# Kernel tuning notes

Measured on AMD Instinct MI355X. Metric: run time of the kernel, lower is better.

## Reference

```python
import jax, jax.numpy as jnp
import numpy as np

N_NODES = 50000
N_EDGES = 1600000
EMB_DIM = 128
HIDDEN = 128   # 2 * out_channels
OUT = 64       # out_channels


def setup_inputs() -> dict:
    key = jax.random.key(0)
    ks = jax.random.split(key, 8)
    x = jnp.arange(N_NODES, dtype=jnp.int64)
    edge_index = jax.random.randint(ks[0], (2, N_EDGES), 0, N_NODES, dtype=jnp.int64)
    emb = jax.random.normal(ks[1], (N_NODES, EMB_DIM), dtype=jnp.float32) * 0.02
    W1 = jax.random.normal(ks[2], (EMB_DIM, HIDDEN), dtype=jnp.float32) / np.sqrt(EMB_DIM).astype(np.float32)
    b1 = jax.random.normal(ks[3], (HIDDEN,), dtype=jnp.float32) * 0.01
    W_mu = jax.random.normal(ks[4], (HIDDEN, OUT), dtype=jnp.float32) / np.sqrt(HIDDEN).astype(np.float32)
    b_mu = jax.random.normal(ks[5], (OUT,), dtype=jnp.float32) * 0.01
    W_logvar = jax.random.normal(ks[6], (HIDDEN, OUT), dtype=jnp.float32) / np.sqrt(HIDDEN).astype(np.float32)
    b_logvar = jax.random.normal(ks[7], (OUT,), dtype=jnp.float32) * 0.01
    return {"x": x, "edge_index": edge_index, "emb": emb, "W1": W1, "b1": b1,
            "W_mu": W_mu, "b_mu": b_mu, "W_logvar": W_logvar, "b_logvar": b_logvar}


def _gcn_norm(edge_index, n_nodes):
    # PyG GCNConv default: add self-loops, symmetric normalization D^-1/2 A D^-1/2
    row, col = edge_index[0], edge_index[1]
    loop = jnp.arange(n_nodes, dtype=row.dtype)
    row = jnp.concatenate([row, loop])  # source nodes
    col = jnp.concatenate([col, loop])  # target nodes (aggregation index)
    deg = jax.ops.segment_sum(jnp.ones_like(col, dtype=jnp.float32), col, num_segments=n_nodes)
    dis = jnp.where(deg > 0, jax.lax.rsqrt(jnp.maximum(deg, 1.0)), 0.0)
    norm = dis[row] * dis[col]  # [E + N]
    return row, col, norm


def _gcn_conv(h, row, col, norm, W, b, n_nodes):
    h = h @ W                               # [N, out]
    msg = h[row] * norm[:, None]            # gather source feats, scale per edge
    out = jax.ops.segment_sum(msg, col, num_segments=n_nodes)  # scatter-add at targets
    return out + b


def reference(x, edge_index, emb, W1, b1, W_mu, b_mu, W_logvar, b_logvar):
    n_nodes = emb.shape[0]
    row, col, norm = _gcn_norm(edge_index, n_nodes)
    h = emb[x]                                                  # embedding lookup
    h = jax.nn.relu(_gcn_conv(h, row, col, norm, W1, b1, n_nodes))
    mu = _gcn_conv(h, row, col, norm, W_mu, b_mu, n_nodes)
    logvar = _gcn_conv(h, row, col, norm, W_logvar, b_logvar, n_nodes)
    return (mu, logvar)
```

## Files before the change

### kernel.cpp

```cpp
#include <hip/hip_runtime.h>
#include <hip/hip_bf16.h>

typedef unsigned int uint32;


__global__ __launch_bounds__(256)
void zero_cnt_kernel(uint32* __restrict__ cnt, int n) {
    int i = blockIdx.x * 256 + threadIdx.x;
    if (i < n) cnt[i] = 0u;
}

__global__ __launch_bounds__(256)
void count_kernel(const int* __restrict__ col, int n_edges, uint32* __restrict__ cnt) {
    int e = blockIdx.x * 256 + threadIdx.x;
    if (e < n_edges) atomicAdd(&cnt[col[e]], 1u);
}

__global__ __launch_bounds__(256)
void scan_blk_kernel(const uint32* __restrict__ cnt, uint32* __restrict__ partial,
                     uint32* __restrict__ blk_sums, int n) {
    __shared__ uint32 sh[256];
    int i = blockIdx.x * 256 + (int)threadIdx.x;
    uint32 v = (i < n) ? cnt[i] : 0u;
    sh[threadIdx.x] = v;
    __syncthreads();
    for (int off = 1; off < 256; off <<= 1) {
        uint32 t = (threadIdx.x >= (unsigned)off) ? sh[threadIdx.x - off] : 0u;
        __syncthreads();
        sh[threadIdx.x] += t;
        __syncthreads();
    }
    if (i < n) partial[i] = sh[threadIdx.x] - v;
    if (threadIdx.x == 255) blk_sums[blockIdx.x] = sh[255];
}

__global__ __launch_bounds__(1024)
void scan_sums_kernel(const uint32* __restrict__ blk_sums, uint32* __restrict__ blk_offs, int nb) {
    __shared__ uint32 sh[1024];
    uint32 v = ((int)threadIdx.x < nb) ? blk_sums[threadIdx.x] : 0u;
    sh[threadIdx.x] = v;
    __syncthreads();
    for (int off = 1; off < 1024; off <<= 1) {
        uint32 t = (threadIdx.x >= (unsigned)off) ? sh[threadIdx.x - off] : 0u;
        __syncthreads();
        sh[threadIdx.x] += t;
        __syncthreads();
    }
    if ((int)threadIdx.x < nb) blk_offs[threadIdx.x] = sh[threadIdx.x] - v;
}

__global__ __launch_bounds__(256)
void scan_add_kernel(const uint32* __restrict__ partial, const uint32* __restrict__ blk_offs,
                     const uint32* __restrict__ cnt, uint32* __restrict__ offs,
                     float* __restrict__ dis, uint32* __restrict__ cursor,
                     int n, int n_edges) {
    int i = blockIdx.x * 256 + (int)threadIdx.x;
    if (i < n) {
        offs[i] = partial[i] + blk_offs[blockIdx.x];
        dis[i] = rsqrtf((float)(cnt[i] + 1u));
        cursor[i] = 0u;
    }
    if (i == 0) offs[n] = (uint32)n_edges;
}

static __device__ __forceinline__ uint32 f32_to_bf16_rne(float f) {
    uint32 u = __float_as_uint(f);
    return (u + 0x7fffu + ((u >> 16) & 1u)) >> 16;
}
static __device__ __forceinline__ float bf16_lo(uint32 v) {
    return __uint_as_float(v << 16);
}
static __device__ __forceinline__ float bf16_hi(uint32 v) {
    return __uint_as_float(v & 0xffff0000u);
}

static __device__ __forceinline__
void gemm_body(int gbid, const float* __restrict__ A, const int* __restrict__ gather,
               const float* __restrict__ W0, const float* __restrict__ W1b,
               int wstride, uint32* __restrict__ out, int n_rows) {
    int grp = threadIdx.x >> 4;
    int c8  = (threadIdx.x & 15) * 8;
    int r0  = gbid * 64 + grp * 4;
    if (r0 >= n_rows) return;

    const float* wb = (c8 < 64) ? (W0 + c8) : (W1b + (c8 - 64));

    const float* ap[4];
    #pragma unroll
    for (int i = 0; i < 4; i++) {
        int r = r0 + i;
        if (r > n_rows - 1) r = n_rows - 1;
        int ra = gather ? gather[r] : r;
        ap[i] = A + (size_t)ra * 128;
    }

    float acc[4][8];
    #pragma unroll
    for (int i = 0; i < 4; i++)
        #pragma unroll
        for (int j = 0; j < 8; j++) acc[i][j] = 0.f;

    for (int k = 0; k < 128; k += 4) {
        float4 av[4];
        #pragma unroll
        for (int i = 0; i < 4; i++) av[i] = *(const float4*)(ap[i] + k);

        const float* w = wb + (size_t)k * wstride;
        #pragma unroll
        for (int kk = 0; kk < 4; kk++) {
            float4 w0 = *(const float4*)(w);
            float4 w1 = *(const float4*)(w + 4);
            #pragma unroll
            for (int i = 0; i < 4; i++) {
                float s = (kk == 0) ? av[i].x : (kk == 1) ? av[i].y
                        : (kk == 2) ? av[i].z : av[i].w;
                acc[i][0] = fmaf(s, w0.x, acc[i][0]);
                acc[i][1] = fmaf(s, w0.y, acc[i][1]);
                acc[i][2] = fmaf(s, w0.z, acc[i][2]);
                acc[i][3] = fmaf(s, w0.w, acc[i][3]);
                acc[i][4] = fmaf(s, w1.x, acc[i][4]);
                acc[i][5] = fmaf(s, w1.y, acc[i][5]);
                acc[i][6] = fmaf(s, w1.z, acc[i][6]);
                acc[i][7] = fmaf(s, w1.w, acc[i][7]);
            }
            w += wstride;
        }
    }

    #pragma unroll
    for (int i = 0; i < 4; i++) {
        int r = r0 + i;
        if (r < n_rows) {
            uint4 pk;
            pk.x = f32_to_bf16_rne(acc[i][0]) | (f32_to_bf16_rne(acc[i][1]) << 16);
            pk.y = f32_to_bf16_rne(acc[i][2]) | (f32_to_bf16_rne(acc[i][3]) << 16);
            pk.z = f32_to_bf16_rne(acc[i][4]) | (f32_to_bf16_rne(acc[i][5]) << 16);
            pk.w = f32_to_bf16_rne(acc[i][6]) | (f32_to_bf16_rne(acc[i][7]) << 16);
            *(uint4*)(out + (size_t)r * 64 + (c8 >> 1)) = pk;
        }
    }
}

__global__ __launch_bounds__(256)
void fill_gemm_kernel(const int* __restrict__ row, const int* __restrict__ col,
                      int n_edges, const uint32* __restrict__ offs,
                      uint32* __restrict__ cursor, uint32* __restrict__ csr,
                      const float* __restrict__ A, const int* __restrict__ gather,
                      const float* __restrict__ W0, const float* __restrict__ W1b,
                      int wstride, uint32* __restrict__ out, int n_rows,
                      int n_gemm_blocks) {
    int bid = blockIdx.x;
    int q = bid / 9, r = bid % 9;
    bool is_gemm = (r == 0) && (q < n_gemm_blocks);
    if (is_gemm) {
        gemm_body(q, A, gather, W0, W1b, wstride, out, n_rows);
    } else {
        int before = q + (r ? 1 : 0);
        if (before > n_gemm_blocks) before = n_gemm_blocks;
        int fid = bid - before;
        int e = fid * 256 + (int)threadIdx.x;
        if (e < n_edges) {
            int c = col[e];
            uint32 p = offs[c] + atomicAdd(&cursor[c], 1u);
            csr[p] = (uint32)row[e];
        }
    }
}

__global__ __launch_bounds__(256)
void gemm_kernel(const float* __restrict__ A,
                 const float* __restrict__ W0, const float* __restrict__ W1b,
                 int wstride, uint32* __restrict__ out, int n_rows) {
    gemm_body(blockIdx.x, A, (const int*)nullptr, W0, W1b, wstride, out, n_rows);
}

__global__ __launch_bounds__(256)
void agg_relu_kernel(const uint32* __restrict__ hs, const uint32* __restrict__ offs,
                     const uint32* __restrict__ csr, const float* __restrict__ dis,
                     const float* __restrict__ bias, float* __restrict__ out, int n_nodes) {
    int wid = (blockIdx.x * 256 + (int)threadIdx.x) >> 6;
    int lane = threadIdx.x & 63;
    if (wid >= n_nodes) return;

    float dv = dis[wid];
    uint32 sv = hs[(size_t)wid * 64 + lane];
    float ax = dv * bf16_lo(sv), ay = dv * bf16_hi(sv);
    int beg = (int)offs[wid], end = (int)offs[wid + 1];

    int j = beg;
    for (; j + 8 <= end; j += 8) {
        uint32 e0 = csr[j],     e1 = csr[j + 1], e2 = csr[j + 2], e3 = csr[j + 3];
        uint32 e4 = csr[j + 4], e5 = csr[j + 5], e6 = csr[j + 6], e7 = csr[j + 7];
        float d0 = dis[e0], d1 = dis[e1], d2 = dis[e2], d3 = dis[e3];
        float d4 = dis[e4], d5 = dis[e5], d6 = dis[e6], d7 = dis[e7];
        uint32 v0 = hs[(size_t)e0 * 64 + lane];
        uint32 v1 = hs[(size_t)e1 * 64 + lane];
        uint32 v2 = hs[(size_t)e2 * 64 + lane];
        uint32 v3 = hs[(size_t)e3 * 64 + lane];
        uint32 v4 = hs[(size_t)e4 * 64 + lane];
        uint32 v5 = hs[(size_t)e5 * 64 + lane];
        uint32 v6 = hs[(size_t)e6 * 64 + lane];
        uint32 v7 = hs[(size_t)e7 * 64 + lane];
        ax = fmaf(d0, bf16_lo(v0), ax); ay = fmaf(d0, bf16_hi(v0), ay);
        ax = fmaf(d1, bf16_lo(v1), ax); ay = fmaf(d1, bf16_hi(v1), ay);
        ax = fmaf(d2, bf16_lo(v2), ax); ay = fmaf(d2, bf16_hi(v2), ay);
        ax = fmaf(d3, bf16_lo(v3), ax); ay = fmaf(d3, bf16_hi(v3), ay);
        ax = fmaf(d4, bf16_lo(v4), ax); ay = fmaf(d4, bf16_hi(v4), ay);
        ax = fmaf(d5, bf16_lo(v5), ax); ay = fmaf(d5, bf16_hi(v5), ay);
        ax = fmaf(d6, bf16_lo(v6), ax); ay = fmaf(d6, bf16_hi(v6), ay);
        ax = fmaf(d7, bf16_lo(v7), ax); ay = fmaf(d7, bf16_hi(v7), ay);
    }
    for (; j < end; ++j) {
        uint32 e = csr[j];
        float d = dis[e];
        uint32 v = hs[(size_t)e * 64 + lane];
        ax = fmaf(d, bf16_lo(v), ax); ay = fmaf(d, bf16_hi(v), ay);
    }

    float2 b = ((const float2*)bias)[lane];
    float2 o;
    o.x = fmaxf(fmaf(dv, ax, b.x), 0.f);
    o.y = fmaxf(fmaf(dv, ay, b.y), 0.f);
    ((float2*)out)[(size_t)wid * 64 + lane] = o;
}

__global__ __launch_bounds__(256)
void agg_out_kernel(const uint32* __restrict__ hs, const uint32* __restrict__ offs,
                    const uint32* __restrict__ csr, const float* __restrict__ dis,
                    const float* __restrict__ bmu, const float* __restrict__ blv,
                    float* __restrict__ out_mu, float* __restrict__ out_lv, int n_nodes) {
    int wid = (blockIdx.x * 256 + (int)threadIdx.x) >> 6;
    int lane = threadIdx.x & 63;
    if (wid >= n_nodes) return;

    float dv = dis[wid];
    uint32 sv = hs[(size_t)wid * 64 + lane];
    float ax = dv * bf16_lo(sv), ay = dv * bf16_hi(sv);
    int beg = (int)offs[wid], end = (int)offs[wid + 1];

    int j = beg;
    for (; j + 8 <= end; j += 8) {
        uint32 e0 = csr[j],     e1 = csr[j + 1], e2 = csr[j + 2], e3 = csr[j + 3];
        uint32 e4 = csr[j + 4], e5 = csr[j + 5], e6 = csr[j + 6], e7 = csr[j + 7];
        float d0 = dis[e0], d1 = dis[e1], d2 = dis[e2], d3 = dis[e3];
        float d4 = dis[e4], d5 = dis[e5], d6 = dis[e6], d7 = dis[e7];
        uint32 v0 = hs[(size_t)e0 * 64 + lane];
        uint32 v1 = hs[(size_t)e1 * 64 + lane];
        uint32 v2 = hs[(size_t)e2 * 64 + lane];
        uint32 v3 = hs[(size_t)e3 * 64 + lane];
        uint32 v4 = hs[(size_t)e4 * 64 + lane];
        uint32 v5 = hs[(size_t)e5 * 64 + lane];
        uint32 v6 = hs[(size_t)e6 * 64 + lane];
        uint32 v7 = hs[(size_t)e7 * 64 + lane];
        ax = fmaf(d0, bf16_lo(v0), ax); ay = fmaf(d0, bf16_hi(v0), ay);
        ax = fmaf(d1, bf16_lo(v1), ax); ay = fmaf(d1, bf16_hi(v1), ay);
        ax = fmaf(d2, bf16_lo(v2), ax); ay = fmaf(d2, bf16_hi(v2), ay);
        ax = fmaf(d3, bf16_lo(v3), ax); ay = fmaf(d3, bf16_hi(v3), ay);
        ax = fmaf(d4, bf16_lo(v4), ax); ay = fmaf(d4, bf16_hi(v4), ay);
        ax = fmaf(d5, bf16_lo(v5), ax); ay = fmaf(d5, bf16_hi(v5), ay);
        ax = fmaf(d6, bf16_lo(v6), ax); ay = fmaf(d6, bf16_hi(v6), ay);
        ax = fmaf(d7, bf16_lo(v7), ax); ay = fmaf(d7, bf16_hi(v7), ay);
    }
    for (; j < end; ++j) {
        uint32 e = csr[j];
        float d = dis[e];
        uint32 v = hs[(size_t)e * 64 + lane];
        ax = fmaf(d, bf16_lo(v), ax); ay = fmaf(d, bf16_hi(v), ay);
    }

    if (lane < 32) {
        float2 b = ((const float2*)bmu)[lane];
        float2 o = make_float2(fmaf(dv, ax, b.x), fmaf(dv, ay, b.y));
        ((float2*)out_mu)[(size_t)wid * 32 + lane] = o;
    } else {
        int l2 = lane - 32;
        float2 b = ((const float2*)blv)[l2];
        float2 o = make_float2(fmaf(dv, ax, b.x), fmaf(dv, ay, b.y));
        ((float2*)out_lv)[(size_t)wid * 32 + l2] = o;
    }
}


extern "C" void kernel_launch(void* const* d_in, const int* in_sizes, int n_in,
                              void* d_out, int out_size, void* d_ws, size_t ws_size,
                              hipStream_t stream) {
    const int*   x   = (const int*)d_in[0];
    const int*   ei  = (const int*)d_in[1];
    const float* emb = (const float*)d_in[2];
    const float* W1  = (const float*)d_in[3];
    const float* b1  = (const float*)d_in[4];
    const float* Wmu = (const float*)d_in[5];
    const float* bmu = (const float*)d_in[6];
    const float* Wlv = (const float*)d_in[7];
    const float* blv = (const float*)d_in[8];

    int n_nodes = in_sizes[0];
    int n_edges = in_sizes[1] / 2;
    const int* row = ei;
    const int* col = ei + n_edges;

    char* wp = (char*)d_ws;
    auto carve = [&wp](size_t bytes) -> char* {
        char* p = wp;
        wp += (bytes + 255) & ~(size_t)255;
        return p;
    };
    int nb = (n_nodes + 255) / 256;

    uint32* cnt     = (uint32*)carve((size_t)n_nodes * 4);
    uint32* cursor  = (uint32*)carve((size_t)n_nodes * 4);
    uint32* offs    = (uint32*)carve(((size_t)n_nodes + 1) * 4);
    uint32* partial = (uint32*)carve((size_t)n_nodes * 4);
    uint32* bsums   = (uint32*)carve((size_t)nb * 4);
    uint32* boffs   = (uint32*)carve((size_t)nb * 4);
    float*  dis     = (float*) carve((size_t)n_nodes * 4);
    uint32* csr     = (uint32*)carve((size_t)n_edges * 4);
    uint32* bufA    = (uint32*)carve((size_t)n_nodes * 64 * 4);
    float*  bufB    = (float*) carve((size_t)n_nodes * 128 * 4);

    int gb_e = (n_edges + 255) / 256;
    int gemm_blocks = (n_nodes + 63) / 64;
    int agg_blocks  = (n_nodes + 3) / 4;

    hipLaunchKernelGGL(zero_cnt_kernel, dim3(nb), dim3(256), 0, stream, cnt, n_nodes);
    hipLaunchKernelGGL(count_kernel, dim3(gb_e), dim3(256), 0, stream, col, n_edges, cnt);
    hipLaunchKernelGGL(scan_blk_kernel, dim3(nb), dim3(256), 0, stream, cnt, partial, bsums, n_nodes);
    hipLaunchKernelGGL(scan_sums_kernel, dim3(1), dim3(1024), 0, stream, bsums, boffs, nb);
    hipLaunchKernelGGL(scan_add_kernel, dim3(nb), dim3(256), 0, stream,
                       partial, boffs, cnt, offs, dis, cursor, n_nodes, n_edges);

    hipLaunchKernelGGL(fill_gemm_kernel, dim3(gb_e + gemm_blocks), dim3(256), 0, stream,
                       row, col, n_edges, offs, cursor, csr,
                       emb, x, W1, W1 + 64, 128, bufA, n_nodes, gemm_blocks);

    hipLaunchKernelGGL(agg_relu_kernel, dim3(agg_blocks), dim3(256), 0, stream,
                       bufA, offs, csr, dis, b1, bufB, n_nodes);

    hipLaunchKernelGGL(gemm_kernel, dim3(gemm_blocks), dim3(256), 0, stream,
                       bufB, Wmu, Wlv, 64, bufA, n_nodes);

    float* out_mu = (float*)d_out;
    float* out_lv = out_mu + (size_t)n_nodes * 64;
    hipLaunchKernelGGL(agg_out_kernel, dim3(agg_blocks), dim3(256), 0, stream,
                       bufA, offs, csr, dis, bmu, blv, out_mu, out_lv, n_nodes);
}
```

Measured before the change: 466.3 us.

## Fuse layer-1 aggregation with second-layer GEMM via shared-memory tile

Replaces the separate layer-1 aggregation kernel (which wrote a 128-wide fp32 hidden buffer) and the follow-up GEMM kernel with one kernel. Each 256-thread block aggregates 32 nodes into LDS, applies bias and ReLU, then multiplies by Wmu/Wlv and writes bf16 results. This removes the fp32 hidden round trip through global memory and one launch. The price is one node per wave processed serially (8 nodes per wave), a block-wide barrier, and a scalar FMA GEMM that reloads weights from global memory. The zeroing kernel is also replaced with hipMemsetAsync.

Result: faster. 453.4 us (-2.8%).

```diff
diff --git a/kernel.cpp b/kernel.cpp
--- a/kernel.cpp
+++ b/kernel.cpp
@@ -3,12 +3,6 @@
 
 typedef unsigned int uint32;
 
-
-__global__ __launch_bounds__(256)
-void zero_cnt_kernel(uint32* __restrict__ cnt, int n) {
-    int i = blockIdx.x * 256 + threadIdx.x;
-    if (i < n) cnt[i] = 0u;
-}
 
 __global__ __launch_bounds__(256)
 void count_kernel(const int* __restrict__ col, int n_edges, uint32* __restrict__ cnt) {
@@ -168,16 +162,113 @@
 }
 
 __global__ __launch_bounds__(256)
-void gemm_kernel(const float* __restrict__ A,
-                 const float* __restrict__ W0, const float* __restrict__ W1b,
-                 int wstride, uint32* __restrict__ out, int n_rows) {
-    gemm_body(blockIdx.x, A, (const int*)nullptr, W0, W1b, wstride, out, n_rows);
-}
-
-__global__ __launch_bounds__(256)
-void agg_relu_kernel(const uint32* __restrict__ hs, const uint32* __restrict__ offs,
-                     const uint32* __restrict__ csr, const float* __restrict__ dis,
-                     const float* __restrict__ bias, float* __restrict__ out, int n_nodes) {
+void agg1_gemm2_kernel(const uint32* __restrict__ hs, const uint32* __restrict__ offs,
+                       const uint32* __restrict__ csr, const float* __restrict__ dis,
+                       const float* __restrict__ b1,
+                       const float* __restrict__ Wmu, const float* __restrict__ Wlv,
+                       uint32* __restrict__ out, int n_nodes) {
+    __shared__ float h1[32][132];
+    int wave = threadIdx.x >> 6;
+    int lane = threadIdx.x & 63;
+    int base = blockIdx.x * 32;
+
+    for (int i = 0; i < 8; i++) {
+        int nl = wave * 8 + i;
+        int wid = base + nl;
+        float ax = 0.f, ay = 0.f;
+        if (wid < n_nodes) {
+            float dv = dis[wid];
+            uint32 sv = hs[(size_t)wid * 64 + lane];
+            ax = dv * bf16_lo(sv); ay = dv * bf16_hi(sv);
+            int beg = (int)offs[wid], end = (int)offs[wid + 1];
+            int j = beg;
+            for (; j + 8 <= end; j += 8) {
+                uint32 e0 = csr[j],     e1 = csr[j + 1], e2 = csr[j + 2], e3 = csr[j + 3];
+                uint32 e4 = csr[j + 4], e5 = csr[j + 5], e6 = csr[j + 6], e7 = csr[j + 7];
+                float d0 = dis[e0], d1 = dis[e1], d2 = dis[e2], d3 = dis[e3];
+                float d4 = dis[e4], d5 = dis[e5], d6 = dis[e6], d7 = dis[e7];
+                uint32 v0 = hs[(size_t)e0 * 64 + lane];
+                uint32 v1 = hs[(size_t)e1 * 64 + lane];
+                uint32 v2 = hs[(size_t)e2 * 64 + lane];
+                uint32 v3 = hs[(size_t)e3 * 64 + lane];
+                uint32 v4 = hs[(size_t)e4 * 64 + lane];
+                uint32 v5 = hs[(size_t)e5 * 64 + lane];
+                uint32 v6 = hs[(size_t)e6 * 64 + lane];
+                uint32 v7 = hs[(size_t)e7 * 64 + lane];
+                ax = fmaf(d0, bf16_lo(v0), ax); ay = fmaf(d0, bf16_hi(v0), ay);
+                ax = fmaf(d1, bf16_lo(v1), ax); ay = fmaf(d1, bf16_hi(v1), ay);
+                ax = fmaf(d2, bf16_lo(v2), ax); ay = fmaf(d2, bf16_hi(v2), ay);
+                ax = fmaf(d3, bf16_lo(v3), ax); ay = fmaf(d3, bf16_hi(v3), ay);
+                ax = fmaf(d4, bf16_lo(v4), ax); ay = fmaf(d4, bf16_hi(v4), ay);
+                ax = fmaf(d5, bf16_lo(v5), ax); ay = fmaf(d5, bf16_hi(v5), ay);
+                ax = fmaf(d6, bf16_lo(v6), ax); ay = fmaf(d6, bf16_hi(v6), ay);
+                ax = fmaf(d7, bf16_lo(v7), ax); ay = fmaf(d7, bf16_hi(v7), ay);
+            }
+            for (; j < end; ++j) {
+                uint32 e = csr[j];
+                float d = dis[e];
+                uint32 v = hs[(size_t)e * 64 + lane];
+                ax = fmaf(d, bf16_lo(v), ax); ay = fmaf(d, bf16_hi(v), ay);
+            }
+            float2 b = ((const float2*)b1)[lane];
+            ax = fmaxf(fmaf(dv, ax, b.x), 0.f);
+            ay = fmaxf(fmaf(dv, ay, b.y), 0.f);
+        }
+        *(float2*)&h1[nl][2 * lane] = make_float2(ax, ay);
+    }
+    __syncthreads();
+
+    int rgrp = threadIdx.x >> 4;
+    int c8   = (threadIdx.x & 15) * 8;
+    const float* wb = (c8 < 64) ? (Wmu + c8) : (Wlv + (c8 - 64));
+
+    float acc[2][8];
+    #pragma unroll
+    for (int i = 0; i < 2; i++)
+        #pragma unroll
+        for (int j = 0; j < 8; j++) acc[i][j] = 0.f;
+
+    for (int k = 0; k < 128; k += 4) {
+        float4 av0 = *(const float4*)&h1[2 * rgrp][k];
+        float4 av1 = *(const float4*)&h1[2 * rgrp + 1][k];
+        const float* w = wb + (size_t)k * 64;
+        #pragma unroll
+        for (int kk = 0; kk < 4; kk++) {
+            float4 w0 = *(const float4*)(w);
+            float4 w1 = *(const float4*)(w + 4);
+            float s0 = (kk == 0) ? av0.x : (kk == 1) ? av0.y : (kk == 2) ? av0.z : av0.w;
+            float s1 = (kk == 0) ? av1.x : (kk == 1) ? av1.y : (kk == 2) ? av1.z : av1.w;
+            acc[0][0] = fmaf(s0, w0.x, acc[0][0]); acc[1][0] = fmaf(s1, w0.x, acc[1][0]);
+            acc[0][1] = fmaf(s0, w0.y, acc[0][1]); acc[1][1] = fmaf(s1, w0.y, acc[1][1]);
+            acc[0][2] = fmaf(s0, w0.z, acc[0][2]); acc[1][2] = fmaf(s1, w0.z, acc[1][2]);
+            acc[0][3] = fmaf(s0, w0.w, acc[0][3]); acc[1][3] = fmaf(s1, w0.w, acc[1][3]);
+            acc[0][4] = fmaf(s0, w1.x, acc[0][4]); acc[1][4] = fmaf(s1, w1.x, acc[1][4]);
+            acc[0][5] = fmaf(s0, w1.y, acc[0][5]); acc[1][5] = fmaf(s1, w1.y, acc[1][5]);
+            acc[0][6] = fmaf(s0, w1.z, acc[0][6]); acc[1][6] = fmaf(s1, w1.z, acc[1][6]);
+            acc[0][7] = fmaf(s0, w1.w, acc[0][7]); acc[1][7] = fmaf(s1, w1.w, acc[1][7]);
+            w += 64;
+        }
+    }
+
+    #pragma unroll
+    for (int i = 0; i < 2; i++) {
+        int r = base + 2 * rgrp + i;
+        if (r < n_nodes) {
+            uint4 pk;
+            pk.x = f32_to_bf16_rne(acc[i][0]) | (f32_to_bf16_rne(acc[i][1]) << 16);
+            pk.y = f32_to_bf16_rne(acc[i][2]) | (f32_to_bf16_rne(acc[i][3]) << 16);
+            pk.z = f32_to_bf16_rne(acc[i][4]) | (f32_to_bf16_rne(acc[i][5]) << 16);
+            pk.w = f32_to_bf16_rne(acc[i][6]) | (f32_to_bf16_rne(acc[i][7]) << 16);
+            *(uint4*)(out + (size_t)r * 64 + (c8 >> 1)) = pk;
+        }
+    }
+}
+
+__global__ __launch_bounds__(256)
+void agg_out_kernel(const uint32* __restrict__ hs, const uint32* __restrict__ offs,
+                    const uint32* __restrict__ csr, const float* __restrict__ dis,
+                    const float* __restrict__ bmu, const float* __restrict__ blv,
+                    float* __restrict__ out_mu, float* __restrict__ out_lv, int n_nodes) {
     int wid = (blockIdx.x * 256 + (int)threadIdx.x) >> 6;
     int lane = threadIdx.x & 63;
     if (wid >= n_nodes) return;
@@ -217,57 +308,6 @@
         ax = fmaf(d, bf16_lo(v), ax); ay = fmaf(d, bf16_hi(v), ay);
     }
 
-    float2 b = ((const float2*)bias)[lane];
-    float2 o;
-    o.x = fmaxf(fmaf(dv, ax, b.x), 0.f);
-    o.y = fmaxf(fmaf(dv, ay, b.y), 0.f);
-    ((float2*)out)[(size_t)wid * 64 + lane] = o;
-}
-
-__global__ __launch_bounds__(256)
-void agg_out_kernel(const uint32* __restrict__ hs, const uint32* __restrict__ offs,
-                    const uint32* __restrict__ csr, const float* __restrict__ dis,
-                    const float* __restrict__ bmu, const float* __restrict__ blv,
-                    float* __restrict__ out_mu, float* __restrict__ out_lv, int n_nodes) {
-    int wid = (blockIdx.x * 256 + (int)threadIdx.x) >> 6;
-    int lane = threadIdx.x & 63;
-    if (wid >= n_nodes) return;
-
-    float dv = dis[wid];
-    uint32 sv = hs[(size_t)wid * 64 + lane];
-    float ax = dv * bf16_lo(sv), ay = dv * bf16_hi(sv);
-    int beg = (int)offs[wid], end = (int)offs[wid + 1];
-
-    int j = beg;
-    for (; j + 8 <= end; j += 8) {
-        uint32 e0 = csr[j],     e1 = csr[j + 1], e2 = csr[j + 2], e3 = csr[j + 3];
-        uint32 e4 = csr[j + 4], e5 = csr[j + 5], e6 = csr[j + 6], e7 = csr[j + 7];
-        float d0 = dis[e0], d1 = dis[e1], d2 = dis[e2], d3 = dis[e3];
-        float d4 = dis[e4], d5 = dis[e5], d6 = dis[e6], d7 = dis[e7];
-        uint32 v0 = hs[(size_t)e0 * 64 + lane];
-        uint32 v1 = hs[(size_t)e1 * 64 + lane];
-        uint32 v2 = hs[(size_t)e2 * 64 + lane];
-        uint32 v3 = hs[(size_t)e3 * 64 + lane];
-        uint32 v4 = hs[(size_t)e4 * 64 + lane];
-        uint32 v5 = hs[(size_t)e5 * 64 + lane];
-        uint32 v6 = hs[(size_t)e6 * 64 + lane];
-        uint32 v7 = hs[(size_t)e7 * 64 + lane];
-        ax = fmaf(d0, bf16_lo(v0), ax); ay = fmaf(d0, bf16_hi(v0), ay);
-        ax = fmaf(d1, bf16_lo(v1), ax); ay = fmaf(d1, bf16_hi(v1), ay);
-        ax = fmaf(d2, bf16_lo(v2), ax); ay = fmaf(d2, bf16_hi(v2), ay);
-        ax = fmaf(d3, bf16_lo(v3), ax); ay = fmaf(d3, bf16_hi(v3), ay);
-        ax = fmaf(d4, bf16_lo(v4), ax); ay = fmaf(d4, bf16_hi(v4), ay);
-        ax = fmaf(d5, bf16_lo(v5), ax); ay = fmaf(d5, bf16_hi(v5), ay);
-        ax = fmaf(d6, bf16_lo(v6), ax); ay = fmaf(d6, bf16_hi(v6), ay);
-        ax = fmaf(d7, bf16_lo(v7), ax); ay = fmaf(d7, bf16_hi(v7), ay);
-    }
-    for (; j < end; ++j) {
-        uint32 e = csr[j];
-        float d = dis[e];
-        uint32 v = hs[(size_t)e * 64 + lane];
-        ax = fmaf(d, bf16_lo(v), ax); ay = fmaf(d, bf16_hi(v), ay);
-    }
-
     if (lane < 32) {
         float2 b = ((const float2*)bmu)[lane];
         float2 o = make_float2(fmaf(dv, ax, b.x), fmaf(dv, ay, b.y));
@@ -316,13 +356,14 @@
     float*  dis     = (float*) carve((size_t)n_nodes * 4);
     uint32* csr     = (uint32*)carve((size_t)n_edges * 4);
     uint32* bufA    = (uint32*)carve((size_t)n_nodes * 64 * 4);
-    float*  bufB    = (float*) carve((size_t)n_nodes * 128 * 4);
+    uint32* bufC    = (uint32*)carve((size_t)n_nodes * 64 * 4);
 
     int gb_e = (n_edges + 255) / 256;
     int gemm_blocks = (n_nodes + 63) / 64;
     int agg_blocks  = (n_nodes + 3) / 4;
-
-    hipLaunchKernelGGL(zero_cnt_kernel, dim3(nb), dim3(256), 0, stream, cnt, n_nodes);
+    int ag_blocks   = (n_nodes + 31) / 32;
+
+    hipMemsetAsync(cnt, 0, (size_t)n_nodes * 4, stream);
     hipLaunchKernelGGL(count_kernel, dim3(gb_e), dim3(256), 0, stream, col, n_edges, cnt);
     hipLaunchKernelGGL(scan_blk_kernel, dim3(nb), dim3(256), 0, stream, cnt, partial, bsums, n_nodes);
     hipLaunchKernelGGL(scan_sums_kernel, dim3(1), dim3(1024), 0, stream, bsums, boffs, nb);
@@ -333,14 +374,11 @@
                        row, col, n_edges, offs, cursor, csr,
                        emb, x, W1, W1 + 64, 128, bufA, n_nodes, gemm_blocks);
 
-    hipLaunchKernelGGL(agg_relu_kernel, dim3(agg_blocks), dim3(256), 0, stream,
-                       bufA, offs, csr, dis, b1, bufB, n_nodes);
-
-    hipLaunchKernelGGL(gemm_kernel, dim3(gemm_blocks), dim3(256), 0, stream,
-                       bufB, Wmu, Wlv, 64, bufA, n_nodes);
+    hipLaunchKernelGGL(agg1_gemm2_kernel, dim3(ag_blocks), dim3(256), 0, stream,
+                       bufA, offs, csr, dis, b1, Wmu, Wlv, bufC, n_nodes);
 
     float* out_mu = (float*)d_out;
     float* out_lv = out_mu + (size_t)n_nodes * 64;
     hipLaunchKernelGGL(agg_out_kernel, dim3(agg_blocks), dim3(256), 0, stream,
-                       bufA, offs, csr, dis, bmu, blv, out_mu, out_lv, n_nodes);
-}
+                       bufC, offs, csr, dis, bmu, blv, out_mu, out_lv, n_nodes);
+}
```
